# Performance work log

Measured on AMD Instinct MI355X. Metric: run time of the kernel, lower is better.

The kernel has to match this reference:

```python
import jax, jax.numpy as jnp
import numpy as np

B, S = 256, 256          # batch, seq_len
V, E = 8000, 128         # char vocab, char emb dim
HC, HW = 128, 256        # char_lstm_hid_dim, word_lstm_hid_dim


def setup_inputs() -> dict:
    key = jax.random.key(0)
    ks = jax.random.split(key, 20)
    n = lambda k, sh: (jax.random.normal(k, sh) * 0.05).astype(jnp.float32)
    return {
        "insts": jax.random.randint(ks[0], (B, S), 0, V),
        "golds": jax.random.randint(ks[1], (B, S), 0, 3),
        "emb": n(ks[2], (V, E)),
        "Wih_f": n(ks[3], (4 * HC, E)), "Whh_f": n(ks[4], (4 * HC, HC)), "b_f": n(ks[5], (4 * HC,)),
        "Wih_b": n(ks[6], (4 * HC, E)), "Whh_b": n(ks[7], (4 * HC, HC)), "b_b": n(ks[8], (4 * HC,)),
        "sub_Wih": n(ks[9], (4 * HW, 2 * HC)), "sub_Whh": n(ks[10], (4 * HW, HW)), "sub_b": n(ks[11], (4 * HW,)),
        "wrd_Wih": n(ks[12], (4 * HW, HW)), "wrd_Whh": n(ks[13], (4 * HW, HW)), "wrd_b": n(ks[14], (4 * HW,)),
        "cls_W": n(ks[15], (2, HW + 2 * HC)), "cls_b": n(ks[16], (2,)),
    }


def _cell(x, h, c, Wih, Whh, b):
    # PyTorch LSTMCell convention: gates ordered i, f, g, o
    g = x @ Wih.T + h @ Whh.T + b
    i, f, gg, o = jnp.split(g, 4, axis=-1)
    c = jax.nn.sigmoid(f) * c + jax.nn.sigmoid(i) * jnp.tanh(gg)
    h = jax.nn.sigmoid(o) * jnp.tanh(c)
    return h, c


def reference(insts, golds, emb, Wih_f, Whh_f, b_f, Wih_b, Whh_b, b_b,
              sub_Wih, sub_Whh, sub_b, wrd_Wih, wrd_Whh, wrd_b, cls_W, cls_b):
    # --- CharEncoder: embedding + BiLSTM, seq-first output [S, B, 2*HC] ---
    x = emb[insts].transpose(1, 0, 2)  # [S, B, E]
    z = jnp.zeros((B, HC), x.dtype)

    def mk_step(Wih, Whh, b):
        def step(hc, xt):
            h, c = _cell(xt, hc[0], hc[1], Wih, Whh, b)
            return (h, c), h
        return step

    _, hf = jax.lax.scan(mk_step(Wih_f, Whh_f, b_f), (z, z), x)
    _, hb = jax.lax.scan(mk_step(Wih_b, Whh_b, b_b), (z, z), x[::-1])
    chars = jnp.concatenate([hf, hb[::-1]], axis=-1)  # [S, B, 2*HC]

    # subword LSTM input at step t is chars[t-1] (zeros at t=0)
    sub_in = jnp.concatenate([jnp.zeros((1, B, 2 * HC), chars.dtype), chars[:-1]], axis=0)

    smap = jnp.array([1, 2, 2], jnp.int32)  # subword_action_map
    wmap = jnp.array([0, 1, 1], jnp.int32)  # word_action_map
    bidx = jnp.arange(B)

    # stacks: read state at pos, write new state at pos+1, then pos += op
    sh = jnp.zeros((2 * S + 2, B, HW), chars.dtype)
    sc = jnp.zeros((2 * S + 2, B, HW), chars.dtype)
    wh = jnp.zeros((S + 1, B, HW), chars.dtype)
    wc = jnp.zeros((S + 1, B, HW), chars.dtype)
    sp = jnp.zeros((B,), jnp.int32)
    wp = jnp.zeros((B,), jnp.int32)

    def step(carry, inp):
        sh, sc, sp, wh, wc, wp = carry
        xs, xc, g = inp  # subword input [B,2HC], classifier char feat [B,2HC], gold op [B]
        h1, c1 = _cell(xs, sh[sp, bidx], sc[sp, bidx], sub_Wih, sub_Whh, sub_b)
        sh = sh.at[sp + 1, bidx].set(h1)
        sc = sc.at[sp + 1, bidx].set(c1)
        h2, c2 = _cell(h1, wh[wp, bidx], wc[wp, bidx], wrd_Wih, wrd_Whh, wrd_b)
        wh = wh.at[wp + 1, bidx].set(h2)
        wc = wc.at[wp + 1, bidx].set(c2)
        out = jnp.concatenate([h2, xc], axis=-1) @ cls_W.T + cls_b  # [B, 2]
        return (sh, sc, sp + smap[g], wh, wc, wp + wmap[g]), out

    _, outs = jax.lax.scan(step, (sh, sc, sp, wh, wc, wp),
                           (sub_in, chars, golds.T.astype(jnp.int32)))
    return outs.transpose(1, 0, 2)  # [B, S, 2]
```

## Files before the change

### kernel.cpp

```cpp
#include <hip/hip_runtime.h>

#define S_LEN 256
#define BATCH 256

typedef _Float16 f16;
typedef _Float16 f16x8 __attribute__((ext_vector_type(8)));
typedef _Float16 f16x4 __attribute__((ext_vector_type(4)));
typedef float f32x4 __attribute__((ext_vector_type(4)));

__device__ inline float sigf(float x) { return 1.f / (1.f + __expf(-x)); }
__device__ inline float tanhf2(float x) { return 2.f * sigf(2.f * x) - 1.f; }

__global__ void k_convert(const float* __restrict__ w3, const float* __restrict__ w4,
                          const float* __restrict__ w6, const float* __restrict__ w7,
                          const float* __restrict__ w9, const float* __restrict__ w10,
                          const float* __restrict__ w12, const float* __restrict__ w13,
                          f16* __restrict__ dst) {
  int i = blockIdx.x * blockDim.x + threadIdx.x;
  const int n = 1310720;
  for (; i < n; i += gridDim.x * blockDim.x) {
    float v;
    if (i < 262144) {
      int m = i >> 16, j = i & 65535;
      v = (m == 0 ? w3 : m == 1 ? w4 : m == 2 ? w6 : w7)[j];
    } else {
      int k = i - 262144;
      int m = k >> 18, j = k & 262143;
      v = (m == 0 ? w9 : m == 1 ? w10 : m == 2 ? w12 : w13)[j];
    }
    dst[i] = (f16)v;
  }
}

__global__ void k_zero(unsigned* __restrict__ p, int n) {
  int i = blockIdx.x * blockDim.x + threadIdx.x;
  for (; i < n; i += gridDim.x * blockDim.x) p[i] = 0u;
}

__global__ void k_gather(const int* __restrict__ insts, const float* __restrict__ emb,
                         f16* __restrict__ Xf) {
  int gid = blockIdx.x * blockDim.x + threadIdx.x;
  int row = gid >> 5;
  int ch = gid & 31;
  int t = row >> 8, b = row & 255;
  int v = insts[b * S_LEN + t];
  const float* src = emb + (size_t)v * 128 + ch * 4;
  f16x4 d;
  d[0] = (f16)src[0]; d[1] = (f16)src[1]; d[2] = (f16)src[2]; d[3] = (f16)src[3];
  *(f16x4*)&Xf[(size_t)row * 128 + ch * 4] = d;
}

__global__ __launch_bounds__(512, 1)
void k_char(const f16* __restrict__ wbuf, const f16* __restrict__ Xf,
            const float* __restrict__ bias_f, const float* __restrict__ bias_b,
            f16* __restrict__ chars) {
  const int bwd = blockIdx.x >> 4;
  const int m0 = (blockIdx.x & 15) * 16;
  const f16* Wih = wbuf + (bwd ? 131072 : 0);
  const f16* Whh = wbuf + (bwd ? 196608 : 65536);
  const float* bias = bwd ? bias_b : bias_f;

  const int tid = threadIdx.x;
  const int lane = tid & 63;
  const int wave = tid >> 6;
  const int gw = wave >> 1;
  const int u0 = (wave & 1) * 64;
  const int l15 = lane & 15;
  const int kb = (lane >> 4) * 8;

  __shared__ f16 xs[2][16][136];
  __shared__ f16 hs[16][136];
  __shared__ float gex[16][520];

  f16x8 fih[4][4], fhh[4][4];
  float bv[4];
#pragma unroll
  for (int tt = 0; tt < 4; ++tt) {
    int col = gw * 128 + u0 + tt * 16 + l15;
    bv[tt] = bias[col];
#pragma unroll
    for (int ks = 0; ks < 4; ++ks) {
      fih[tt][ks] = *(const f16x8*)&Wih[col * 128 + ks * 32 + kb];
      fhh[tt][ks] = *(const f16x8*)&Whh[col * 128 + ks * 32 + kb];
    }
  }

  for (int i = tid; i < 16 * 136; i += 512) ((f16*)hs)[i] = (f16)0.f;
  {
    int mm = tid >> 5, cc = (tid & 31) * 4;
    int t_in = bwd ? (S_LEN - 1) : 0;
    *(f16x4*)&xs[0][mm][cc] =
        *(const f16x4*)&Xf[(size_t)t_in * BATCH * 128 + (m0 + mm) * 128 + cc];
  }
  float cst[4] = {0.f, 0.f, 0.f, 0.f};
  const int cm = tid >> 5;
  const int cu = (tid & 31) * 4;
  __syncthreads();

  for (int s = 0; s < S_LEN; ++s) {
    const int par = s & 1;
    f32x4 acc[4];
#pragma unroll
    for (int tt = 0; tt < 4; ++tt) { f32x4 a = {bv[tt], bv[tt], bv[tt], bv[tt]}; acc[tt] = a; }
#pragma unroll
    for (int ks = 0; ks < 4; ++ks) {
      f16x8 ax = *(const f16x8*)&xs[par][l15][ks * 32 + kb];
      f16x8 ah = *(const f16x8*)&hs[l15][ks * 32 + kb];
#pragma unroll
      for (int tt = 0; tt < 4; ++tt) {
        acc[tt] = __builtin_amdgcn_mfma_f32_16x16x32_f16(ax, fih[tt][ks], acc[tt], 0, 0, 0);
        acc[tt] = __builtin_amdgcn_mfma_f32_16x16x32_f16(ah, fhh[tt][ks], acc[tt], 0, 0, 0);
      }
    }
    f16x4 xreg;
    const int sn = s + 1;
    if (sn < S_LEN) {
      int t_in = bwd ? (S_LEN - 1 - sn) : sn;
      xreg = *(const f16x4*)&Xf[(size_t)t_in * BATCH * 128 + (m0 + cm) * 128 + cu];
    }
#pragma unroll
    for (int tt = 0; tt < 4; ++tt) {
      int col = gw * 128 + u0 + tt * 16 + l15;
#pragma unroll
      for (int r = 0; r < 4; ++r) gex[(lane >> 4) * 4 + r][col] = acc[tt][r];
    }
    __syncthreads();
    f16x4 hv;
#pragma unroll
    for (int qq = 0; qq < 4; ++qq) {
      int u = cu + qq;
      float gi = gex[cm][u], gf = gex[cm][128 + u], gg = gex[cm][256 + u], go = gex[cm][384 + u];
      float c = sigf(gf) * cst[qq] + sigf(gi) * tanhf2(gg);
      cst[qq] = c;
      hv[qq] = (f16)(sigf(go) * tanhf2(c));
    }
    {
      int t_in = bwd ? (S_LEN - 1 - s) : s;
      int cbase = bwd ? (128 + cu) : cu;
      *(f16x4*)&chars[(size_t)t_in * BATCH * 256 + (m0 + cm) * 256 + cbase] = hv;
      *(f16x4*)&hs[cm][cu] = hv;
      if (sn < S_LEN) *(f16x4*)&xs[par ^ 1][cm][cu] = xreg;
    }
    __syncthreads();
  }
}

__global__ __launch_bounds__(256, 1)
void k_subword(const f16* __restrict__ wbuf, const f16* __restrict__ chars,
               const int* __restrict__ golds,
               const float* __restrict__ b_sub, const float* __restrict__ b_wrd,
               f16* __restrict__ h1buf, f16* __restrict__ whbuf,
               unsigned* __restrict__ flags, f16* __restrict__ H2) {
  const int team = blockIdx.x >> 4;
  const int q = blockIdx.x & 15;
  const int m0 = team * 16;
  const int h0 = q * 16;
  const int tid = threadIdx.x, lane = tid & 63, wave = tid >> 6;
  const int l15 = lane & 15, kb = (lane >> 4) * 8;

  const f16* sWih = wbuf + 262144;
  const f16* sWhh = wbuf + 524288;
  const f16* wWih = wbuf + 786432;
  const f16* wWhh = wbuf + 1048576;

  __shared__ f16 xs_s[16][264];
  __shared__ f16 h1_s[16][264];
  __shared__ f16 wh_s[16][264];
  __shared__ float gexS[16][68];
  __shared__ float gexW[16][68];
  __shared__ int golds_s[16][256];

  f16x8 fsi[8], fsh[8], fwi[8], fwh[8];
  const int wr = wave * 256 + h0 + l15;
#pragma unroll
  for (int ks = 0; ks < 8; ++ks) {
    fsi[ks] = *(const f16x8*)&sWih[wr * 256 + ks * 32 + kb];
    fsh[ks] = *(const f16x8*)&sWhh[wr * 256 + ks * 32 + kb];
    fwi[ks] = *(const f16x8*)&wWih[wr * 256 + ks * 32 + kb];
    fwh[ks] = *(const f16x8*)&wWhh[wr * 256 + ks * 32 + kb];
  }
  const float bS = b_sub[wr], bW = b_wrd[wr];

  for (int i = tid; i < 16 * 256; i += 256)
    golds_s[i >> 8][i & 255] = golds[(m0 + (i >> 8)) * S_LEN + (i & 255)];
  for (int i = tid; i < 16 * 264; i += 256) {
    ((f16*)xs_s)[i] = (f16)0.f;
    ((f16*)h1_s)[i] = (f16)0.f;
    ((f16*)wh_s)[i] = (f16)0.f;
  }
  const int cm = tid >> 4, cj = tid & 15;
  const int sr = tid >> 4;
  const int sc = (tid & 15) * 16;
  float c_sub = 0.f, c_wrd = 0.f;
  __syncthreads();

  for (int i = 0; i <= S_LEN; ++i) {
    const bool doW = (i > 0), doS = (i < S_LEN);

    f16x4 chpre[4];
    if (doS) {
#pragma unroll
      for (int p = 0; p < 4; ++p)
        chpre[p] = *(const f16x4*)&chars[(size_t)i * BATCH * 256 + (m0 + sr) * 256 + sc + p * 4];
    }

    f32x4 accW = {bW, bW, bW, bW};
    f32x4 accS = {bS, bS, bS, bS};
    if (doW) {
#pragma unroll
      for (int ks = 0; ks < 8; ++ks) {
        f16x8 a1 = *(const f16x8*)&h1_s[l15][ks * 32 + kb];
        f16x8 aw = *(const f16x8*)&wh_s[l15][ks * 32 + kb];
        accW = __builtin_amdgcn_mfma_f32_16x16x32_f16(a1, fwi[ks], accW, 0, 0, 0);
        accW = __builtin_amdgcn_mfma_f32_16x16x32_f16(aw, fwh[ks], accW, 0, 0, 0);
      }
    }
    if (doS) {
      const bool keep = (i > 0) && (golds_s[l15][i > 0 ? i - 1 : 0] == 0);
      f16x8 z8 = {};
#pragma unroll
      for (int ks = 0; ks < 8; ++ks) {
        f16x8 axv = *(const f16x8*)&xs_s[l15][ks * 32 + kb];
        f16x8 a1 = *(const f16x8*)&h1_s[l15][ks * 32 + kb];
        a1 = keep ? a1 : z8;
        accS = __builtin_amdgcn_mfma_f32_16x16x32_f16(axv, fsi[ks], accS, 0, 0, 0);
        accS = __builtin_amdgcn_mfma_f32_16x16x32_f16(a1, fsh[ks], accS, 0, 0, 0);
      }
    }
#pragma unroll
    for (int r = 0; r < 4; ++r) {
      if (doW) gexW[(lane >> 4) * 4 + r][wave * 16 + l15] = accW[r];
      if (doS) gexS[(lane >> 4) * 4 + r][wave * 16 + l15] = accS[r];
    }
    __syncthreads();

    const int gprev = (i > 0) ? golds_s[cm][i - 1] : 1;
    if (doW) {
      float gi = gexW[cm][cj], gf = gexW[cm][16 + cj], gg = gexW[cm][32 + cj],
            go = gexW[cm][48 + cj];
      float c2 = sigf(gf) * c_wrd + sigf(gi) * tanhf2(gg);
      float h2 = sigf(go) * tanhf2(c2);
      bool adv = (gprev != 0);
      if (adv) c_wrd = c2;
      float whold = (float)wh_s[cm][h0 + cj];
      f16 whnew = (f16)(adv ? h2 : whold);
      H2[(size_t)(i - 1) * BATCH * 256 + (m0 + cm) * 256 + h0 + cj] = (f16)h2;
      if (doS)
        __hip_atomic_store(
            (unsigned short*)&whbuf[(size_t)(i & 1) * 65536 + (m0 + cm) * 256 + h0 + cj],
            __builtin_bit_cast(unsigned short, whnew), __ATOMIC_RELAXED,
            __HIP_MEMORY_SCOPE_AGENT);
    }
    if (doS) {
      float gi = gexS[cm][cj], gf = gexS[cm][16 + cj], gg = gexS[cm][32 + cj],
            go = gexS[cm][48 + cj];
      float cp = (gprev == 0) ? c_sub : 0.f;
      float c1 = sigf(gf) * cp + sigf(gi) * tanhf2(gg);
      c_sub = c1;
      f16 h1 = (f16)(sigf(go) * tanhf2(c1));
      __hip_atomic_store(
          (unsigned short*)&h1buf[(size_t)(i & 1) * 65536 + (m0 + cm) * 256 + h0 + cj],
          __builtin_bit_cast(unsigned short, h1), __ATOMIC_RELAXED, __HIP_MEMORY_SCOPE_AGENT);
    }
    __syncthreads();

    if (doS) {
      if (tid == 0)
        __hip_atomic_store(&flags[(team * 16 + q) * 16], (unsigned)(i + 1), __ATOMIC_RELAXED,
                           __HIP_MEMORY_SCOPE_AGENT);
      if (tid < 64) {
        const unsigned tgt = (unsigned)(i + 1);
        while (true) {
          unsigned v = tgt;
          if (lane < 16)
            v = __hip_atomic_load(&flags[(team * 16 + lane) * 16], __ATOMIC_RELAXED,
                                  __HIP_MEMORY_SCOPE_AGENT);
          if (__all(v >= tgt)) break;
          __builtin_amdgcn_s_sleep(1);
        }
      }
      asm volatile("" ::: "memory");
      __syncthreads();
#pragma unroll
      for (int p = 0; p < 4; ++p) {
        int c4 = sc + p * 4;
        unsigned long long v1 = __hip_atomic_load(
            (const unsigned long long*)&h1buf[(size_t)(i & 1) * 65536 + (m0 + sr) * 256 + c4],
            __ATOMIC_RELAXED, __HIP_MEMORY_SCOPE_AGENT);
        unsigned long long v2 = __hip_atomic_load(
            (const unsigned long long*)&whbuf[(size_t)(i & 1) * 65536 + (m0 + sr) * 256 + c4],
            __ATOMIC_RELAXED, __HIP_MEMORY_SCOPE_AGENT);
        *(f16x4*)&h1_s[sr][c4] = __builtin_bit_cast(f16x4, v1);
        *(f16x4*)&wh_s[sr][c4] = __builtin_bit_cast(f16x4, v2);
        *(f16x4*)&xs_s[sr][c4] = chpre[p];
      }
      __syncthreads();
    }
  }
}

__global__ __launch_bounds__(256)
void k_cls(const f16* __restrict__ H2, const f16* __restrict__ chars,
           const float* __restrict__ clsW, const float* __restrict__ clsb,
           float* __restrict__ out) {
  const int w = (blockIdx.x << 2) | (threadIdx.x >> 6);
  const int lane = threadIdx.x & 63;
  const int t = w >> 8, b = w & 255;
  const f16* h2p = H2 + (size_t)w * 256;
  const f16* chp = chars + (size_t)w * 256;
  float s0 = 0.f, s1 = 0.f;
  f16x4 hv = *(const f16x4*)&h2p[lane * 4];
  f16x4 cv = *(const f16x4*)&chp[lane * 4];
#pragma unroll
  for (int qq = 0; qq < 4; ++qq) {
    int u = lane * 4 + qq;
    s0 += (float)hv[qq] * clsW[u] + (float)cv[qq] * clsW[256 + u];
    s1 += (float)hv[qq] * clsW[512 + u] + (float)cv[qq] * clsW[768 + u];
  }
#pragma unroll
  for (int off = 32; off >= 1; off >>= 1) {
    s0 += __shfl_down(s0, off);
    s1 += __shfl_down(s1, off);
  }
  if (lane == 0) {
    out[((size_t)b * S_LEN + t) * 2 + 0] = s0 + clsb[0];
    out[((size_t)b * S_LEN + t) * 2 + 1] = s1 + clsb[1];
  }
}

extern "C" void kernel_launch(void* const* d_in, const int* in_sizes, int n_in,
                              void* d_out, int out_size, void* d_ws, size_t ws_size,
                              hipStream_t stream) {
  const int* insts = (const int*)d_in[0];
  const int* golds = (const int*)d_in[1];
  const float* emb = (const float*)d_in[2];
  const float* wihf = (const float*)d_in[3];
  const float* whhf = (const float*)d_in[4];
  const float* bf = (const float*)d_in[5];
  const float* wihb = (const float*)d_in[6];
  const float* whhb = (const float*)d_in[7];
  const float* bb = (const float*)d_in[8];
  const float* swih = (const float*)d_in[9];
  const float* swhh = (const float*)d_in[10];
  const float* sb = (const float*)d_in[11];
  const float* wwih = (const float*)d_in[12];
  const float* wwhh = (const float*)d_in[13];
  const float* wb = (const float*)d_in[14];
  const float* clsW = (const float*)d_in[15];
  const float* clsb = (const float*)d_in[16];
  float* out = (float*)d_out;

  const size_t OFF_W = 0;
  const size_t OFF_XF = 2621440;
  const size_t OFF_CHARS = 19398656;
  const size_t OFF_H2 = 52953088;
  const size_t OFF_H1 = 86507520;
  const size_t OFF_WH = 86769664;
  const size_t OFF_FLAGS = 87031808;
  const size_t TOTAL = 87048192;
  if (ws_size < TOTAL) return;

  char* ws = (char*)d_ws;
  f16* wbuf = (f16*)(ws + OFF_W);
  f16* Xf = (f16*)(ws + OFF_XF);
  f16* chars = (f16*)(ws + OFF_CHARS);
  f16* H2 = (f16*)(ws + OFF_H2);
  f16* h1buf = (f16*)(ws + OFF_H1);
  f16* whbuf = (f16*)(ws + OFF_WH);
  unsigned* flags = (unsigned*)(ws + OFF_FLAGS);

  hipLaunchKernelGGL(k_convert, dim3(1024), dim3(256), 0, stream, wihf, whhf, wihb, whhb,
                     swih, swhh, wwih, wwhh, wbuf);
  hipLaunchKernelGGL(k_zero, dim3(256), dim3(256), 0, stream, (unsigned*)(ws + OFF_H1),
                     135168);
  hipLaunchKernelGGL(k_gather, dim3(8192), dim3(256), 0, stream, insts, emb, Xf);
  hipLaunchKernelGGL(k_char, dim3(32), dim3(512), 0, stream, wbuf, Xf, bf, bb, chars);
  hipLaunchKernelGGL(k_subword, dim3(256), dim3(256), 0, stream, wbuf, chars, golds, sb, wb,
                     h1buf, whbuf, flags, H2);
  hipLaunchKernelGGL(k_cls, dim3(16384), dim3(256), 0, stream, H2, chars, clsW, clsb, out);
}
```

Before: 1.370 ms.

## Replace flag barrier with tagged per-value publication in subword recurrence

The subword kernel drops its separate flag array and per-team barrier. Each published h1/wh value is now stored as a 32-bit word tagged with the step number, and each consumer thread spins only on the words it needs. Blocks are reshaped to 512 threads covering 32 hidden units, which halves the grid to 128 blocks, and the word hidden state is kept in a register. Register-pinning asm and f32x4 weight storage are added to both recurrent kernels. This trades a flag round-trip and an extra barrier per step for twice the publication traffic and more polling loads.

```diff
diff --git a/kernel.cpp b/kernel.cpp
--- a/kernel.cpp
+++ b/kernel.cpp
@@ -50,7 +50,7 @@
   *(f16x4*)&Xf[(size_t)row * 128 + ch * 4] = d;
 }
 
-__global__ __launch_bounds__(512, 1)
+__global__ __launch_bounds__(512, 2)
 void k_char(const f16* __restrict__ wbuf, const f16* __restrict__ Xf,
             const float* __restrict__ bias_f, const float* __restrict__ bias_b,
             f16* __restrict__ chars) {
@@ -72,7 +72,7 @@
   __shared__ f16 hs[16][136];
   __shared__ float gex[16][520];
 
-  f16x8 fih[4][4], fhh[4][4];
+  f32x4 fih[4][4], fhh[4][4];
   float bv[4];
 #pragma unroll
   for (int tt = 0; tt < 4; ++tt) {
@@ -80,8 +80,8 @@
     bv[tt] = bias[col];
 #pragma unroll
     for (int ks = 0; ks < 4; ++ks) {
-      fih[tt][ks] = *(const f16x8*)&Wih[col * 128 + ks * 32 + kb];
-      fhh[tt][ks] = *(const f16x8*)&Whh[col * 128 + ks * 32 + kb];
+      fih[tt][ks] = *(const f32x4*)&Wih[col * 128 + ks * 32 + kb];
+      fhh[tt][ks] = *(const f32x4*)&Whh[col * 128 + ks * 32 + kb];
     }
   }
 
@@ -98,6 +98,12 @@
   __syncthreads();
 
   for (int s = 0; s < S_LEN; ++s) {
+#pragma unroll
+    for (int tt = 0; tt < 4; ++tt)
+#pragma unroll
+      for (int ks = 0; ks < 4; ++ks)
+        asm volatile("" : "+v"(fih[tt][ks]), "+v"(fhh[tt][ks]));
+
     const int par = s & 1;
     f32x4 acc[4];
 #pragma unroll
@@ -108,8 +114,10 @@
       f16x8 ah = *(const f16x8*)&hs[l15][ks * 32 + kb];
 #pragma unroll
       for (int tt = 0; tt < 4; ++tt) {
-        acc[tt] = __builtin_amdgcn_mfma_f32_16x16x32_f16(ax, fih[tt][ks], acc[tt], 0, 0, 0);
-        acc[tt] = __builtin_amdgcn_mfma_f32_16x16x32_f16(ah, fhh[tt][ks], acc[tt], 0, 0, 0);
+        acc[tt] = __builtin_amdgcn_mfma_f32_16x16x32_f16(
+            ax, __builtin_bit_cast(f16x8, fih[tt][ks]), acc[tt], 0, 0, 0);
+        acc[tt] = __builtin_amdgcn_mfma_f32_16x16x32_f16(
+            ah, __builtin_bit_cast(f16x8, fhh[tt][ks]), acc[tt], 0, 0, 0);
       }
     }
     f16x4 xreg;
@@ -145,18 +153,20 @@
   }
 }
 
-__global__ __launch_bounds__(256, 1)
+__global__ __launch_bounds__(512, 2)
 void k_subword(const f16* __restrict__ wbuf, const f16* __restrict__ chars,
                const int* __restrict__ golds,
                const float* __restrict__ b_sub, const float* __restrict__ b_wrd,
-               f16* __restrict__ h1buf, f16* __restrict__ whbuf,
-               unsigned* __restrict__ flags, f16* __restrict__ H2) {
-  const int team = blockIdx.x >> 4;
-  const int q = blockIdx.x & 15;
+               unsigned* __restrict__ h1pub, unsigned* __restrict__ whpub,
+               f16* __restrict__ H2) {
+  const int team = blockIdx.x & 15;
+  const int q = blockIdx.x >> 4;
   const int m0 = team * 16;
-  const int h0 = q * 16;
+  const int h0 = q * 32;
   const int tid = threadIdx.x, lane = tid & 63, wave = tid >> 6;
   const int l15 = lane & 15, kb = (lane >> 4) * 8;
+  const int g = wave >> 1;
+  const int us = wave & 1;
 
   const f16* sWih = wbuf + 262144;
   const f16* sWhh = wbuf + 524288;
@@ -166,43 +176,45 @@
   __shared__ f16 xs_s[16][264];
   __shared__ f16 h1_s[16][264];
   __shared__ f16 wh_s[16][264];
-  __shared__ float gexS[16][68];
-  __shared__ float gexW[16][68];
-  __shared__ int golds_s[16][256];
-
-  f16x8 fsi[8], fsh[8], fwi[8], fwh[8];
-  const int wr = wave * 256 + h0 + l15;
+  __shared__ float gexS[16][130];
+  __shared__ float gexW[16][130];
+  __shared__ unsigned char golds_s[16][256];
+
+  f32x4 fsi[8], fsh[8], fwi[8], fwh[8];
+  const int wr = g * 256 + h0 + us * 16 + l15;
 #pragma unroll
   for (int ks = 0; ks < 8; ++ks) {
-    fsi[ks] = *(const f16x8*)&sWih[wr * 256 + ks * 32 + kb];
-    fsh[ks] = *(const f16x8*)&sWhh[wr * 256 + ks * 32 + kb];
-    fwi[ks] = *(const f16x8*)&wWih[wr * 256 + ks * 32 + kb];
-    fwh[ks] = *(const f16x8*)&wWhh[wr * 256 + ks * 32 + kb];
+    fsi[ks] = *(const f32x4*)&sWih[wr * 256 + ks * 32 + kb];
+    fsh[ks] = *(const f32x4*)&sWhh[wr * 256 + ks * 32 + kb];
+    fwi[ks] = *(const f32x4*)&wWih[wr * 256 + ks * 32 + kb];
+    fwh[ks] = *(const f32x4*)&wWhh[wr * 256 + ks * 32 + kb];
   }
   const float bS = b_sub[wr], bW = b_wrd[wr];
 
-  for (int i = tid; i < 16 * 256; i += 256)
-    golds_s[i >> 8][i & 255] = golds[(m0 + (i >> 8)) * S_LEN + (i & 255)];
-  for (int i = tid; i < 16 * 264; i += 256) {
-    ((f16*)xs_s)[i] = (f16)0.f;
-    ((f16*)h1_s)[i] = (f16)0.f;
-    ((f16*)wh_s)[i] = (f16)0.f;
-  }
-  const int cm = tid >> 4, cj = tid & 15;
-  const int sr = tid >> 4;
-  const int sc = (tid & 15) * 16;
-  float c_sub = 0.f, c_wrd = 0.f;
+  for (int j = tid; j < 16 * 256; j += 512)
+    golds_s[j >> 8][j & 255] = (unsigned char)golds[(m0 + (j >> 8)) * S_LEN + (j & 255)];
+  for (int j = tid; j < 16 * 264; j += 512) {
+    ((f16*)xs_s)[j] = (f16)0.f;
+    ((f16*)h1_s)[j] = (f16)0.f;
+    ((f16*)wh_s)[j] = (f16)0.f;
+  }
+  const int cb = tid >> 5, cu = tid & 31;
+  const int sr = tid >> 5;
+  const int c0 = (tid & 31) * 8;
+  float c_sub = 0.f, c_wrd = 0.f, wh_reg = 0.f;
   __syncthreads();
 
   for (int i = 0; i <= S_LEN; ++i) {
     const bool doW = (i > 0), doS = (i < S_LEN);
-
-    f16x4 chpre[4];
-    if (doS) {
-#pragma unroll
-      for (int p = 0; p < 4; ++p)
-        chpre[p] = *(const f16x4*)&chars[(size_t)i * BATCH * 256 + (m0 + sr) * 256 + sc + p * 4];
-    }
+    const int slotbase = ((i & 1) * 16 + team) << 12;
+
+#pragma unroll
+    for (int ks = 0; ks < 8; ++ks)
+      asm volatile("" : "+v"(fsi[ks]), "+v"(fsh[ks]), "+v"(fwi[ks]), "+v"(fwh[ks]));
+
+    f16x8 chpre;
+    if (doS)
+      chpre = *(const f16x8*)&chars[(size_t)i * BATCH * 256 + (m0 + sr) * 256 + c0];
 
     f32x4 accW = {bW, bW, bW, bW};
     f32x4 accS = {bS, bS, bS, bS};
@@ -211,8 +223,10 @@
       for (int ks = 0; ks < 8; ++ks) {
         f16x8 a1 = *(const f16x8*)&h1_s[l15][ks * 32 + kb];
         f16x8 aw = *(const f16x8*)&wh_s[l15][ks * 32 + kb];
-        accW = __builtin_amdgcn_mfma_f32_16x16x32_f16(a1, fwi[ks], accW, 0, 0, 0);
-        accW = __builtin_amdgcn_mfma_f32_16x16x32_f16(aw, fwh[ks], accW, 0, 0, 0);
+        accW = __builtin_amdgcn_mfma_f32_16x16x32_f16(
+            a1, __builtin_bit_cast(f16x8, fwi[ks]), accW, 0, 0, 0);
+        accW = __builtin_amdgcn_mfma_f32_16x16x32_f16(
+            aw, __builtin_bit_cast(f16x8, fwh[ks]), accW, 0, 0, 0);
       }
     }
     if (doS) {
@@ -223,77 +237,82 @@
         f16x8 axv = *(const f16x8*)&xs_s[l15][ks * 32 + kb];
         f16x8 a1 = *(const f16x8*)&h1_s[l15][ks * 32 + kb];
         a1 = keep ? a1 : z8;
-        accS = __builtin_amdgcn_mfma_f32_16x16x32_f16(axv, fsi[ks], accS, 0, 0, 0);
-        accS = __builtin_amdgcn_mfma_f32_16x16x32_f16(a1, fsh[ks], accS, 0, 0, 0);
+        accS = __builtin_amdgcn_mfma_f32_16x16x32_f16(
+            axv, __builtin_bit_cast(f16x8, fsi[ks]), accS, 0, 0, 0);
+        accS = __builtin_amdgcn_mfma_f32_16x16x32_f16(
+            a1, __builtin_bit_cast(f16x8, fsh[ks]), accS, 0, 0, 0);
       }
     }
 #pragma unroll
     for (int r = 0; r < 4; ++r) {
-      if (doW) gexW[(lane >> 4) * 4 + r][wave * 16 + l15] = accW[r];
-      if (doS) gexS[(lane >> 4) * 4 + r][wave * 16 + l15] = accS[r];
+      int row = (lane >> 4) * 4 + r;
+      int colp = g * 32 + us * 16 + l15;
+      if (doW) gexW[row][colp] = accW[r];
+      if (doS) gexS[row][colp] = accS[r];
     }
     __syncthreads();
 
-    const int gprev = (i > 0) ? golds_s[cm][i - 1] : 1;
+    const int gprev = (i > 0) ? (int)golds_s[cb][i - 1] : 1;
+    f16 h1v = (f16)0.f;
     if (doW) {
-      float gi = gexW[cm][cj], gf = gexW[cm][16 + cj], gg = gexW[cm][32 + cj],
-            go = gexW[cm][48 + cj];
+      float gi = gexW[cb][cu], gf = gexW[cb][32 + cu], gg = gexW[cb][64 + cu],
+            go = gexW[cb][96 + cu];
       float c2 = sigf(gf) * c_wrd + sigf(gi) * tanhf2(gg);
       float h2 = sigf(go) * tanhf2(c2);
       bool adv = (gprev != 0);
-      if (adv) c_wrd = c2;
-      float whold = (float)wh_s[cm][h0 + cj];
-      f16 whnew = (f16)(adv ? h2 : whold);
-      H2[(size_t)(i - 1) * BATCH * 256 + (m0 + cm) * 256 + h0 + cj] = (f16)h2;
-      if (doS)
-        __hip_atomic_store(
-            (unsigned short*)&whbuf[(size_t)(i & 1) * 65536 + (m0 + cm) * 256 + h0 + cj],
-            __builtin_bit_cast(unsigned short, whnew), __ATOMIC_RELAXED,
-            __HIP_MEMORY_SCOPE_AGENT);
+      if (adv) { c_wrd = c2; wh_reg = h2; }
+      H2[(size_t)(i - 1) * BATCH * 256 + (m0 + cb) * 256 + h0 + cu] = (f16)h2;
     }
     if (doS) {
-      float gi = gexS[cm][cj], gf = gexS[cm][16 + cj], gg = gexS[cm][32 + cj],
-            go = gexS[cm][48 + cj];
+      float gi = gexS[cb][cu], gf = gexS[cb][32 + cu], gg = gexS[cb][64 + cu],
+            go = gexS[cb][96 + cu];
       float cp = (gprev == 0) ? c_sub : 0.f;
       float c1 = sigf(gf) * cp + sigf(gi) * tanhf2(gg);
       c_sub = c1;
-      f16 h1 = (f16)(sigf(go) * tanhf2(c1));
-      __hip_atomic_store(
-          (unsigned short*)&h1buf[(size_t)(i & 1) * 65536 + (m0 + cm) * 256 + h0 + cj],
-          __builtin_bit_cast(unsigned short, h1), __ATOMIC_RELAXED, __HIP_MEMORY_SCOPE_AGENT);
-    }
-    __syncthreads();
+      h1v = (f16)(sigf(go) * tanhf2(c1));
+      const unsigned tag = (unsigned)(i + 1) << 16;
+      const int pidx = slotbase + cb * 256 + h0 + cu;
+      __hip_atomic_store(&h1pub[pidx],
+                         tag | (unsigned)__builtin_bit_cast(unsigned short, h1v),
+                         __ATOMIC_RELAXED, __HIP_MEMORY_SCOPE_AGENT);
+      __hip_atomic_store(&whpub[pidx],
+                         tag | (unsigned)__builtin_bit_cast(unsigned short, (f16)wh_reg),
+                         __ATOMIC_RELAXED, __HIP_MEMORY_SCOPE_AGENT);
+    }
 
     if (doS) {
-      if (tid == 0)
-        __hip_atomic_store(&flags[(team * 16 + q) * 16], (unsigned)(i + 1), __ATOMIC_RELAXED,
-                           __HIP_MEMORY_SCOPE_AGENT);
-      if (tid < 64) {
-        const unsigned tgt = (unsigned)(i + 1);
-        while (true) {
-          unsigned v = tgt;
-          if (lane < 16)
-            v = __hip_atomic_load(&flags[(team * 16 + lane) * 16], __ATOMIC_RELAXED,
-                                  __HIP_MEMORY_SCOPE_AGENT);
-          if (__all(v >= tgt)) break;
-          __builtin_amdgcn_s_sleep(1);
+      asm volatile("" ::: "memory");
+      const unsigned tgt = (unsigned)(i + 1);
+      const int base = slotbase + sr * 256 + c0;
+      unsigned hw[8], ww[8];
+#pragma unroll
+      for (int k = 0; k < 8; ++k) { hw[k] = 0u; ww[k] = 0u; }
+      while (true) {
+        bool ok = true;
+#pragma unroll
+        for (int k = 0; k < 8; ++k) {
+          if ((hw[k] >> 16) != tgt) {
+            hw[k] = __hip_atomic_load(&h1pub[base + k], __ATOMIC_RELAXED,
+                                      __HIP_MEMORY_SCOPE_AGENT);
+            ok &= ((hw[k] >> 16) == tgt);
+          }
+          if ((ww[k] >> 16) != tgt) {
+            ww[k] = __hip_atomic_load(&whpub[base + k], __ATOMIC_RELAXED,
+                                      __HIP_MEMORY_SCOPE_AGENT);
+            ok &= ((ww[k] >> 16) == tgt);
+          }
         }
-      }
-      asm volatile("" ::: "memory");
-      __syncthreads();
-#pragma unroll
-      for (int p = 0; p < 4; ++p) {
-        int c4 = sc + p * 4;
-        unsigned long long v1 = __hip_atomic_load(
-            (const unsigned long long*)&h1buf[(size_t)(i & 1) * 65536 + (m0 + sr) * 256 + c4],
-            __ATOMIC_RELAXED, __HIP_MEMORY_SCOPE_AGENT);
-        unsigned long long v2 = __hip_atomic_load(
-            (const unsigned long long*)&whbuf[(size_t)(i & 1) * 65536 + (m0 + sr) * 256 + c4],
-            __ATOMIC_RELAXED, __HIP_MEMORY_SCOPE_AGENT);
-        *(f16x4*)&h1_s[sr][c4] = __builtin_bit_cast(f16x4, v1);
-        *(f16x4*)&wh_s[sr][c4] = __builtin_bit_cast(f16x4, v2);
-        *(f16x4*)&xs_s[sr][c4] = chpre[p];
-      }
+        if (ok) break;
+      }
+      union { unsigned u[4]; f16x8 v; } uh, uw;
+#pragma unroll
+      for (int k2 = 0; k2 < 4; ++k2) {
+        uh.u[k2] = (hw[2 * k2] & 0xffffu) | (hw[2 * k2 + 1] << 16);
+        uw.u[k2] = (ww[2 * k2] & 0xffffu) | (ww[2 * k2 + 1] << 16);
+      }
+      *(f16x8*)&h1_s[sr][c0] = uh.v;
+      *(f16x8*)&wh_s[sr][c0] = uw.v;
+      *(f16x8*)&xs_s[sr][c0] = chpre;
       __syncthreads();
     }
   }
@@ -352,11 +371,10 @@
 
   const size_t OFF_W = 0;
   const size_t OFF_XF = 2621440;
+  const size_t OFF_PUBH1 = OFF_XF + 4194304;
+  const size_t OFF_PUBWH = OFF_PUBH1 + 524288;
   const size_t OFF_CHARS = 19398656;
   const size_t OFF_H2 = 52953088;
-  const size_t OFF_H1 = 86507520;
-  const size_t OFF_WH = 86769664;
-  const size_t OFF_FLAGS = 87031808;
   const size_t TOTAL = 87048192;
   if (ws_size < TOTAL) return;
 
@@ -365,17 +383,16 @@
   f16* Xf = (f16*)(ws + OFF_XF);
   f16* chars = (f16*)(ws + OFF_CHARS);
   f16* H2 = (f16*)(ws + OFF_H2);
-  f16* h1buf = (f16*)(ws + OFF_H1);
-  f16* whbuf = (f16*)(ws + OFF_WH);
-  unsigned* flags = (unsigned*)(ws + OFF_FLAGS);
+  unsigned* h1pub = (unsigned*)(ws + OFF_PUBH1);
+  unsigned* whpub = (unsigned*)(ws + OFF_PUBWH);
 
   hipLaunchKernelGGL(k_convert, dim3(1024), dim3(256), 0, stream, wihf, whhf, wihb, whhb,
                      swih, swhh, wwih, wwhh, wbuf);
-  hipLaunchKernelGGL(k_zero, dim3(256), dim3(256), 0, stream, (unsigned*)(ws + OFF_H1),
-                     135168);
   hipLaunchKernelGGL(k_gather, dim3(8192), dim3(256), 0, stream, insts, emb, Xf);
   hipLaunchKernelGGL(k_char, dim3(32), dim3(512), 0, stream, wbuf, Xf, bf, bb, chars);
-  hipLaunchKernelGGL(k_subword, dim3(256), dim3(256), 0, stream, wbuf, chars, golds, sb, wb,
-                     h1buf, whbuf, flags, H2);
+  hipLaunchKernelGGL(k_zero, dim3(512), dim3(256), 0, stream, (unsigned*)(ws + OFF_PUBH1),
+                     262144);
+  hipLaunchKernelGGL(k_subword, dim3(128), dim3(512), 0, stream, wbuf, chars, golds, sb, wb,
+                     h1pub, whpub, H2);
   hipLaunchKernelGGL(k_cls, dim3(16384), dim3(256), 0, stream, H2, chars, clsW, clsb, out);
 }
```

Result: slower. 2.244 ms (+63.8%).
